# Performance work log

Measured on AMD Instinct MI355X. Metric: run time of the kernel, lower is better.

## Reference

```python
import jax, jax.numpy as jnp
import numpy as np

B, T, C = 4, 2048, 1024   # batch, seq (block_size), n_embd
H, D = 16, 64             # num_heads, head_size (H*D == C)


def setup_inputs() -> dict:
    key = jax.random.key(0)
    ks = jax.random.split(key, 6)
    s = 0.02
    return {
        "x":  jax.random.normal(ks[0], (B, T, C), jnp.float32),
        "Wq": jax.random.normal(ks[1], (H, C, D), jnp.float32) * s,
        "Wk": jax.random.normal(ks[2], (H, C, D), jnp.float32) * s,
        "Wv": jax.random.normal(ks[3], (H, C, D), jnp.float32) * s,
        "Wp": jax.random.normal(ks[4], (C, C), jnp.float32) * s,
        "bp": jnp.zeros((C,), jnp.float32),
        "is_masked": 1,
    }


def reference(x, Wq, Wk, Wv, Wp, bp, is_masked):
    # Batched per-head projections (original loops over H separate Linears)
    q = jnp.einsum("btc,hcd->bhtd", x, Wq)
    k = jnp.einsum("btc,hcd->bhtd", x, Wk)
    v = jnp.einsum("btc,hcd->bhtd", x, Wv)
    # NOTE: original divides by sqrt(C) where C = n_embd (input dim), not head_size
    scores = jnp.einsum("bhtd,bhsd->bhts", q, k) / jnp.sqrt(jnp.asarray(C, x.dtype))
    if is_masked:
        causal = jnp.tril(jnp.ones((T, T), bool))
        scores = jnp.where(causal, scores, jnp.asarray(-jnp.inf, scores.dtype))
    attn = jax.nn.softmax(scores, axis=-1)   # dropout is identity in eval mode
    out = jnp.einsum("bhts,bhsd->bhtd", attn, v)
    # concat heads along the last dim: [B,T,H*D] == [B,T,C]
    out = out.transpose(0, 2, 1, 3).reshape(B, T, C)
    return out @ Wp.T + bp
```

## Files before the change

### kernel.cpp

```cpp
#include <hip/hip_runtime.h>
#include <stdint.h>
#include <type_traits>

typedef unsigned short u16;
typedef unsigned int u32;
typedef __attribute__((ext_vector_type(8))) short frag8;
typedef __attribute__((ext_vector_type(4))) float fx4;
typedef __attribute__((ext_vector_type(16))) float fx16;

#define MFMA(a, b, c) __builtin_amdgcn_mfma_f32_16x16x32_bf16((a), (b), (c), 0, 0, 0)
#define MFMA32(a, b, c) __builtin_amdgcn_mfma_f32_32x32x16_bf16((a), (b), (c), 0, 0, 0)

__device__ __forceinline__ void gload16(const void* g, void* l) {
  __builtin_amdgcn_global_load_lds((const __attribute__((address_space(1))) void*)g,
                                   (__attribute__((address_space(3))) void*)l, 16, 0, 0);
}

__device__ __forceinline__ u16 f2bf(float f) {
  union { float f; unsigned int u; } c; c.f = f;
  unsigned int r = c.u + 0x7FFFu + ((c.u >> 16) & 1u);
  return (u16)(r >> 16);
}

__device__ __forceinline__ u32 cvtpk(float lo, float hi) {
  u32 r;
  asm("v_cvt_pk_bf16_f32 %0, %1, %2" : "=v"(r) : "v"(lo), "v"(hi));
  return r;
}


__global__ __launch_bounds__(256) void cvt_x(const float* __restrict__ x, u16* __restrict__ xb) {
  const int n4 = (8192 * 1024) / 4;
  for (int i = blockIdx.x * 256 + threadIdx.x; i < n4; i += 2048 * 256) {
    float4 v = ((const float4*)x)[i];
    ushort4 o;
    o.x = f2bf(v.x); o.y = f2bf(v.y); o.z = f2bf(v.z); o.w = f2bf(v.w);
    ((ushort4*)xb)[i] = o;
  }
}

__global__ __launch_bounds__(256) void cvt_wqkv(const float* __restrict__ Wq,
                                                const float* __restrict__ Wk,
                                                const float* __restrict__ Wv,
                                                u16* __restrict__ Wt) {
  __shared__ u16 Tls[64][72];
  int hh = blockIdx.x;
  int c0 = blockIdx.y * 64;
  int type = hh >> 4, h = hh & 15;
  const float* Wsrc = (type == 0 ? Wq : (type == 1 ? Wk : Wv)) + (size_t)h * 1024 * 64;
  int t = threadIdx.x;
  int cr = t >> 4, q4 = (t & 15) * 4;
  for (int i = 0; i < 4; ++i) {
    int c = cr + i * 16;
    float4 v = *(const float4*)(Wsrc + (size_t)(c0 + c) * 64 + q4);
    Tls[q4 + 0][c] = f2bf(v.x);
    Tls[q4 + 1][c] = f2bf(v.y);
    Tls[q4 + 2][c] = f2bf(v.z);
    Tls[q4 + 3][c] = f2bf(v.w);
  }
  __syncthreads();
  for (int i = 0; i < 4; ++i) {
    int d = cr + i * 16;
    ushort4 o;
    o.x = Tls[d][q4 + 0]; o.y = Tls[d][q4 + 1]; o.z = Tls[d][q4 + 2]; o.w = Tls[d][q4 + 3];
    *(ushort4*)(Wt + ((size_t)hh * 64 + d) * 1024 + c0 + q4) = o;
  }
}

__global__ __launch_bounds__(256) void cvt_wp(const float* __restrict__ Wp, u16* __restrict__ wb) {
  const int n4 = (1024 * 1024) / 4;
  for (int i = blockIdx.x * 256 + threadIdx.x; i < n4; i += 1024 * 256) {
    float4 v = ((const float4*)Wp)[i];
    ushort4 o;
    o.x = f2bf(v.x); o.y = f2bf(v.y); o.z = f2bf(v.z); o.w = f2bf(v.w);
    ((ushort4*)wb)[i] = o;
  }
}

__global__ __launch_bounds__(256) void transpose_v(const u16* __restrict__ Vb, u16* __restrict__ VTg) {
  __shared__ u16 T[64 * 64];
  int bh = blockIdx.x, t0 = blockIdx.y * 64;
  const u16* src = Vb + ((size_t)bh * 2048 + t0) * 64;
  int tid = threadIdx.x;
  int tl = tid >> 2, c16 = (tid & 3) * 16;
  int swzw = (tl & 7) << 4;
  frag8 a = *(const frag8*)(src + (size_t)tl * 64 + c16);
  frag8 b = *(const frag8*)(src + (size_t)tl * 64 + c16 + 8);
  *(frag8*)((char*)T + tl * 128 + ((c16 * 2) ^ swzw)) = a;
  *(frag8*)((char*)T + tl * 128 + ((c16 * 2 + 16) ^ swzw)) = b;
  __syncthreads();
  int d_ = tid & 63;
#pragma unroll
  for (int k = 0; k < 2; ++k) {
    int c_ = (tid >> 6) + 4 * k;
    frag8 o;
#pragma unroll
    for (int j = 0; j < 8; ++j) {
      int t = c_ * 8 + j;
      o[j] = *(const u16*)((const char*)T + t * 128 + ((2 * d_) ^ ((t & 7) << 4)));
    }
    *(frag8*)(VTg + ((size_t)bh * 64 + d_) * 2048 + t0 + c_ * 8) = o;
  }
}


template <int MODE>
__global__ __launch_bounds__(256) void gemm_bt(const u16* __restrict__ A, const u16* __restrict__ Bw,
                                               u16* __restrict__ Qb, u16* __restrict__ Kb,
                                               u16* __restrict__ Vb, float* __restrict__ outp,
                                               const float* __restrict__ bp) {
  __shared__ u16 As[128 * 32];
  __shared__ u16 Bs[128 * 32];
  int tid = threadIdx.x;
  int m0 = blockIdx.x * 128, n0 = blockIdx.y * 128;
  int wid = tid >> 6, lane = tid & 63, lr = lane & 15, lg = lane >> 4;
  int wm = (wid >> 1) * 64, wn = (wid & 1) * 64;
  const u16* Ag = A + (size_t)m0 * 1024;
  const u16* Bg = Bw + (size_t)n0 * 1024;
  int cidx0 = wid * 2, cidx1 = wid * 2 + 1;
  int rA0 = cidx0 * 16 + (lane >> 2), rA1 = cidx1 * 16 + (lane >> 2);
  int chm = ((lane & 3) ^ ((lane >> 2) & 3)) * 8;
  const u16* Asrc0 = Ag + (size_t)rA0 * 1024 + chm;
  const u16* Asrc1 = Ag + (size_t)rA1 * 1024 + chm;
  const u16* Bsrc0 = Bg + (size_t)rA0 * 1024 + chm;
  const u16* Bsrc1 = Bg + (size_t)rA1 * 1024 + chm;
  u16* lA0 = As + cidx0 * 512; u16* lA1 = As + cidx1 * 512;
  u16* lB0 = Bs + cidx0 * 512; u16* lB1 = Bs + cidx1 * 512;
  int aoff[4], boff[4];
#pragma unroll
  for (int i = 0; i < 4; ++i) {
    aoff[i] = (wm + i * 16 + lr) * 64 + ((lg * 16) ^ ((lr & 3) << 4));
    boff[i] = (wn + i * 16 + lr) * 64 + ((lg * 16) ^ ((lr & 3) << 4));
  }
  fx4 acc[4][4] = {};
  for (int kt = 0; kt < 32; ++kt) {
    __syncthreads();
    gload16(Asrc0 + kt * 32, lA0);
    gload16(Asrc1 + kt * 32, lA1);
    gload16(Bsrc0 + kt * 32, lB0);
    gload16(Bsrc1 + kt * 32, lB1);
    __syncthreads();
    frag8 af[4], bf_[4];
#pragma unroll
    for (int i = 0; i < 4; ++i) af[i] = *(const frag8*)((const char*)As + aoff[i]);
#pragma unroll
    for (int i = 0; i < 4; ++i) bf_[i] = *(const frag8*)((const char*)Bs + boff[i]);
#pragma unroll
    for (int mi = 0; mi < 4; ++mi)
#pragma unroll
      for (int ni = 0; ni < 4; ++ni) acc[mi][ni] = MFMA(af[mi], bf_[ni], acc[mi][ni]);
  }
#pragma unroll
  for (int mi = 0; mi < 4; ++mi)
#pragma unroll
    for (int r = 0; r < 4; ++r) {
      int m = m0 + wm + mi * 16 + lg * 4 + r;
      if (MODE == 0) {
        int b = m >> 11, t = m & 2047;
#pragma unroll
        for (int ni = 0; ni < 4; ++ni) {
          int n = n0 + wn + ni * 16 + lr;
          int type = n >> 10, h = (n >> 6) & 15, d = n & 63;
          u16* dst = (type == 0) ? Qb : ((type == 1) ? Kb : Vb);
          float v = acc[mi][ni][r];
          if (type == 0) v *= 0.04508422002778011f;
          dst[((size_t)(b * 16 + h) * 2048 + t) * 64 + d] = f2bf(v);
        }
      } else {
#pragma unroll
        for (int ni = 0; ni < 4; ++ni) {
          int n = n0 + wn + ni * 16 + lr;
          outp[(size_t)m * 1024 + n] = acc[mi][ni][r] + bp[n];
        }
      }
    }
}


__global__ __launch_bounds__(256, 4) void attn(const u16* __restrict__ Qb, const u16* __restrict__ Kb,
                                               const u16* __restrict__ VTg, u16* __restrict__ Ao,
                                               const int* __restrict__ mflag) {
  __shared__ __align__(16) char LDS[32768];
  const int tid = threadIdx.x, w = tid >> 6, lane = tid & 63;
  const int l31 = lane & 31, hi = lane >> 5;
  const int bh = blockIdx.x;
  const int qt = 15 - (int)blockIdx.y;
  const int masked = mflag[0];
  const int qbase = qt * 128;
  const u16* Qh = Qb + (size_t)bh * (2048 * 64);
  const u16* Kh = Kb + (size_t)bh * (2048 * 64);
  const u16* Vh = VTg + (size_t)bh * (64 * 2048);
  const int qrow = qbase + w * 32 + l31;
  frag8 qf[4];
#pragma unroll
  for (int s = 0; s < 4; ++s) qf[s] = *(const frag8*)(Qh + (size_t)qrow * 64 + s * 16 + hi * 8);
  const int srow = lane >> 3;
  const int schunk = ((lane & 7) ^ srow) * 8;
  const int c0 = w * 2, c1 = w * 2 + 1;
  const u16* kg0 = Kh + (size_t)(c0 * 8 + srow) * 64 + schunk;
  const u16* kg1 = Kh + (size_t)(c1 * 8 + srow) * 64 + schunk;
  const u16* vg0 = Vh + (size_t)(c0 * 8 + srow) * 2048 + schunk;
  const u16* vg1 = Vh + (size_t)(c1 * 8 + srow) * 2048 + schunk;
  const int aK = l31 * 128 + ((hi * 16) ^ ((l31 & 7) << 4));
  const int qmax_w = qbase + w * 32 + 31;
  const int qmin_w = qbase + w * 32;
  float m_run = -__builtin_inff(), l_run = 0.f;
  fx16 oa0 = {}, oa1 = {};
  const int nt = masked ? (2 * qt + 2) : 32;

  auto STAGE = [&](int B, int T) {
    size_t ko = (size_t)T * 4096, vo = (size_t)T * 64;
    gload16(kg0 + ko, LDS + B * 8192 + c0 * 1024);
    gload16(kg1 + ko, LDS + B * 8192 + c1 * 1024);
    gload16(vg0 + vo, LDS + 16384 + B * 8192 + c0 * 1024);
    gload16(vg1 + vo, LDS + 16384 + B * 8192 + c1 * 1024);
  };

  auto TILE = [&](auto Bc, int T) {
    constexpr int B = decltype(Bc)::value;
    if (T + 1 < nt) STAGE(B ^ 1, T + 1);
    bool act = (!masked) || (T * 64 <= qmax_w);
    if (act) {
      fx16 s0v = {}, s1v = {};
#pragma unroll
      for (int ds = 0; ds < 4; ++ds) {
        frag8 k0 = *(const frag8*)(LDS + B * 8192 + (aK ^ (ds << 5)));
        frag8 k1 = *(const frag8*)(LDS + B * 8192 + 4096 + (aK ^ (ds << 5)));
        s0v = MFMA32(k0, qf[ds], s0v);
        s1v = MFMA32(k1, qf[ds], s1v);
      }
      if (masked && T * 64 + 63 > qmin_w) {
#pragma unroll
        for (int g = 0; g < 4; ++g)
#pragma unroll
          for (int r = 0; r < 4; ++r) {
            int sg = T * 64 + r + 8 * g + 4 * hi;
            if (sg > qrow) s0v[4 * g + r] = -__builtin_inff();
            if (sg + 32 > qrow) s1v[4 * g + r] = -__builtin_inff();
          }
      }
      float mx = s0v[0];
#pragma unroll
      for (int i = 1; i < 16; ++i) mx = fmaxf(mx, s0v[i]);
#pragma unroll
      for (int i = 0; i < 16; ++i) mx = fmaxf(mx, s1v[i]);
      mx = fmaxf(mx, __int_as_float(__shfl_xor(__float_as_int(mx), 32)));
      if (!__all(mx <= m_run + 8.0f)) {
        float mn = fmaxf(m_run, mx);
        float al = __builtin_amdgcn_exp2f(m_run - mn);
#pragma unroll
        for (int i = 0; i < 16; ++i) { oa0[i] *= al; oa1[i] *= al; }
        l_run *= al;
        m_run = mn;
      }
      float ps = 0.f;
#pragma unroll
      for (int i = 0; i < 16; ++i) {
        s0v[i] = __builtin_amdgcn_exp2f(s0v[i] - m_run); ps += s0v[i];
      }
#pragma unroll
      for (int i = 0; i < 16; ++i) {
        s1v[i] = __builtin_amdgcn_exp2f(s1v[i] - m_run); ps += s1v[i];
      }
      ps += __int_as_float(__shfl_xor(__float_as_int(ps), 32));
      l_run += ps;
#pragma unroll
      for (int kt = 0; kt < 4; ++kt) {
        const int b8 = (kt & 1) * 8;
        float p0, p1, p2, p3, p4, p5, p6, p7;
        if (kt < 2) { p0=s0v[b8+0];p1=s0v[b8+1];p2=s0v[b8+2];p3=s0v[b8+3];p4=s0v[b8+4];p5=s0v[b8+5];p6=s0v[b8+6];p7=s0v[b8+7]; }
        else        { p0=s1v[b8+0];p1=s1v[b8+1];p2=s1v[b8+2];p3=s1v[b8+3];p4=s1v[b8+4];p5=s1v[b8+5];p6=s1v[b8+6];p7=s1v[b8+7]; }
        u32 X0 = cvtpk(p0, p1), X1 = cvtpk(p2, p3);
        u32 Y0 = cvtpk(p4, p5), Y1 = cvtpk(p6, p7);
        u32 sel0 = hi ? X0 : Y0, sel1 = hi ? X1 : Y1;
        u32 got0 = (u32)__shfl_xor((int)sel0, 32);
        u32 got1 = (u32)__shfl_xor((int)sel1, 32);
        union { u32 u[4]; frag8 f; } pf;
        pf.u[0] = hi ? got0 : X0;
        pf.u[1] = hi ? got1 : X1;
        pf.u[2] = hi ? Y0 : got0;
        pf.u[3] = hi ? Y1 : got1;
        frag8 v0 = *(const frag8*)(LDS + 16384 + B * 8192 + (aK ^ (kt << 5)));
        frag8 v1 = *(const frag8*)(LDS + 16384 + B * 8192 + 4096 + (aK ^ (kt << 5)));
        oa0 = MFMA32(v0, pf.f, oa0);
        oa1 = MFMA32(v1, pf.f, oa1);
      }
    }
    asm volatile("s_waitcnt vmcnt(0)" ::: "memory");
    __builtin_amdgcn_s_barrier();
  };

  STAGE(0, 0);
  asm volatile("s_waitcnt vmcnt(0)" ::: "memory");
  __builtin_amdgcn_s_barrier();
  int t = 0;
  while (true) {
    TILE(std::integral_constant<int, 0>{}, t); ++t; if (t >= nt) break;
    TILE(std::integral_constant<int, 1>{}, t); ++t; if (t >= nt) break;
  }

  float inv = 1.0f / l_run;
  int b = bh >> 4, hh = bh & 15;
  u16* orow = Ao + ((size_t)b * 2048 + qrow) * 1024 + hh * 64;
#pragma unroll
  for (int g = 0; g < 4; ++g) {
    int d0 = 8 * g + 4 * hi;
    u32 wA = cvtpk(oa0[4 * g + 0] * inv, oa0[4 * g + 1] * inv);
    u32 wB = cvtpk(oa0[4 * g + 2] * inv, oa0[4 * g + 3] * inv);
    u32 wC = cvtpk(oa1[4 * g + 0] * inv, oa1[4 * g + 1] * inv);
    u32 wD = cvtpk(oa1[4 * g + 2] * inv, oa1[4 * g + 3] * inv);
    *(u32*)(orow + d0 + 0) = wA;
    *(u32*)(orow + d0 + 2) = wB;
    *(u32*)(orow + d0 + 32) = wC;
    *(u32*)(orow + d0 + 34) = wD;
  }
}


extern "C" void kernel_launch(void* const* d_in, const int* in_sizes, int n_in,
                              void* d_out, int out_size, void* d_ws, size_t ws_size,
                              hipStream_t stream) {
  const float* x = (const float*)d_in[0];
  const float* Wq = (const float*)d_in[1];
  const float* Wk = (const float*)d_in[2];
  const float* Wv = (const float*)d_in[3];
  const float* Wp = (const float*)d_in[4];
  const float* bp = (const float*)d_in[5];
  const int* is_masked = (const int*)d_in[6];
  float* out = (float*)d_out;
  char* ws = (char*)d_ws;
  u16* Xbf = (u16*)(ws + 0);
  u16* Wt  = (u16*)(ws + 16777216);
  u16* Wpb = (u16*)(ws + 23068672);
  u16* Qb  = (u16*)(ws + 25165824);
  u16* Kb  = (u16*)(ws + 41943040);
  u16* Vb  = (u16*)(ws + 58720256);
  u16* Ao  = (u16*)(ws + 75497472);
  u16* VTg = Xbf;

  cvt_x<<<2048, 256, 0, stream>>>(x, Xbf);
  cvt_wqkv<<<dim3(48, 16), 256, 0, stream>>>(Wq, Wk, Wv, Wt);
  cvt_wp<<<1024, 256, 0, stream>>>(Wp, Wpb);
  gemm_bt<0><<<dim3(64, 24), 256, 0, stream>>>(Xbf, Wt, Qb, Kb, Vb, nullptr, nullptr);
  transpose_v<<<dim3(64, 32), 256, 0, stream>>>(Vb, VTg);
  attn<<<dim3(64, 16), 256, 0, stream>>>(Qb, Kb, VTg, Ao, is_masked);
  gemm_bt<1><<<dim3(64, 8), 256, 0, stream>>>(Ao, Wpb, nullptr, nullptr, nullptr, out, bp);
}
```

Before: 168.7 us.

## Replace QKV projection GEMM with 256x192-tile double-buffered 8-wave kernel

The fused QKV projection GEMM moves to a new kernel with 256x192 output tiles, 512 threads, a 64-wide K step and double-buffered LDS filled by direct global-to-LDS loads. Each tile's next K slice is prefetched while MFMAs run, with wave priority raised around the MFMA bursts. Blocks are remapped so neighbouring tiles land on the same XCD, aiming at better L2 reuse. The aim is to raise arithmetic intensity and hide load latency for the biggest GEMM. The cost is 112KB of LDS per block, so fewer blocks fit per CU, and an epilogue with scattered bf16 stores.

```diff
diff --git a/kernel.cpp b/kernel.cpp
--- a/kernel.cpp
+++ b/kernel.cpp
@@ -104,11 +104,115 @@
 }
 
 
-template <int MODE>
-__global__ __launch_bounds__(256) void gemm_bt(const u16* __restrict__ A, const u16* __restrict__ Bw,
-                                               u16* __restrict__ Qb, u16* __restrict__ Kb,
-                                               u16* __restrict__ Vb, float* __restrict__ outp,
-                                               const float* __restrict__ bp) {
+__global__ __launch_bounds__(512, 2) void gemm256(const u16* __restrict__ A, const u16* __restrict__ Bw,
+                                                  u16* __restrict__ Qb, u16* __restrict__ Kb,
+                                                  u16* __restrict__ Vb) {
+  __shared__ __align__(16) char LDSC[114688];
+  const int tid = threadIdx.x, w = tid >> 6, lane = tid & 63;
+  const int lr = lane & 15, lg = lane >> 4;
+  const int wg = blockIdx.x;
+  const int xcd = wg & 7, loc = wg >> 3;
+  const int bx = xcd * 4 + (loc >> 4);
+  const int by = loc & 15;
+  const int m0 = bx * 256, n0 = by * 192;
+  const int r8 = lane >> 3;
+  const int c8 = ((lane & 7) ^ r8) * 8;
+  const u16* aS[4]; const u16* bS[3];
+  char* aD[4]; char* bD[3];
+#pragma unroll
+  for (int l = 0; l < 4; ++l) {
+    aS[l] = A + (size_t)(m0 + l * 64 + w * 8 + r8) * 1024 + c8;
+    aD[l] = LDSC + l * 8192 + w * 1024;
+  }
+#pragma unroll
+  for (int l = 0; l < 3; ++l) {
+    bS[l] = Bw + (size_t)(n0 + l * 64 + w * 8 + r8) * 1024 + c8;
+    bD[l] = LDSC + 65536 + l * 8192 + w * 1024;
+  }
+  const int colX0 = (lg << 4) ^ ((lr & 7) << 4);
+  const int colX1 = ((4 + lg) << 4) ^ ((lr & 7) << 4);
+  const int aRowB = ((w >> 2) * 128 + lr) * 128;
+  const int bRowB = 65536 + ((w & 3) * 48 + lr) * 128;
+
+  fx4 acc[8][3] = {};
+
+#pragma unroll
+  for (int l = 0; l < 4; ++l) gload16(aS[l], aD[l]);
+#pragma unroll
+  for (int l = 0; l < 3; ++l) gload16(bS[l], bD[l]);
+  asm volatile("s_waitcnt vmcnt(0)" ::: "memory");
+  __builtin_amdgcn_s_barrier();
+
+  for (int kt = 0; kt < 16; ++kt) {
+    const int ab = (kt & 1) * 32768;
+    const int bb = (kt & 1) * 24576;
+    frag8 bf2[3][2];
+#pragma unroll
+    for (int p = 0; p < 4; ++p) {
+      if (p == 0) {
+        if (kt + 1 < 16) {
+          const int ko = (kt + 1) * 64;
+          const int ab2 = ab ^ 32768, bb2 = bb ^ 24576;
+#pragma unroll
+          for (int l = 0; l < 4; ++l) gload16(aS[l] + ko, aD[l] + ab2);
+#pragma unroll
+          for (int l = 0; l < 3; ++l) gload16(bS[l] + ko, bD[l] + bb2);
+        }
+#pragma unroll
+        for (int ni = 0; ni < 3; ++ni) {
+          bf2[ni][0] = *(const frag8*)(LDSC + bb + bRowB + ni * 2048 + colX0);
+          bf2[ni][1] = *(const frag8*)(LDSC + bb + bRowB + ni * 2048 + colX1);
+        }
+      }
+      frag8 af2[2][2];
+#pragma unroll
+      for (int dm = 0; dm < 2; ++dm) {
+        af2[dm][0] = *(const frag8*)(LDSC + ab + aRowB + (2 * p + dm) * 2048 + colX0);
+        af2[dm][1] = *(const frag8*)(LDSC + ab + aRowB + (2 * p + dm) * 2048 + colX1);
+      }
+      __builtin_amdgcn_s_barrier();
+      asm volatile("s_waitcnt lgkmcnt(0)" ::: "memory");
+      __builtin_amdgcn_sched_barrier(0);
+      __builtin_amdgcn_s_setprio(1);
+#pragma unroll
+      for (int dm = 0; dm < 2; ++dm)
+#pragma unroll
+        for (int ni = 0; ni < 3; ++ni)
+#pragma unroll
+          for (int ks = 0; ks < 2; ++ks)
+            acc[2 * p + dm][ni] = MFMA(af2[dm][ks], bf2[ni][ks], acc[2 * p + dm][ni]);
+      __builtin_amdgcn_s_setprio(0);
+      __builtin_amdgcn_sched_barrier(0);
+      if (p == 3) {
+        asm volatile("s_waitcnt vmcnt(0)" ::: "memory");
+        __builtin_amdgcn_sched_barrier(0);
+      }
+      __builtin_amdgcn_s_barrier();
+    }
+  }
+
+  const int wmB = (w >> 2) * 128, wnB = (w & 3) * 48;
+#pragma unroll
+  for (int mi = 0; mi < 8; ++mi)
+#pragma unroll
+    for (int r = 0; r < 4; ++r) {
+      int m = m0 + wmB + mi * 16 + lg * 4 + r;
+      int b = m >> 11, t = m & 2047;
+#pragma unroll
+      for (int ni = 0; ni < 3; ++ni) {
+        int n = n0 + wnB + ni * 16 + lr;
+        int type = n >> 10, h = (n >> 6) & 15, d = n & 63;
+        u16* dst = (type == 0) ? Qb : ((type == 1) ? Kb : Vb);
+        float v = acc[mi][ni][r];
+        if (type == 0) v *= 0.04508422002778011f;
+        dst[((size_t)(b * 16 + h) * 2048 + t) * 64 + d] = f2bf(v);
+      }
+    }
+}
+
+
+__global__ __launch_bounds__(256) void gemm_proj(const u16* __restrict__ A, const u16* __restrict__ Bw,
+                                                 float* __restrict__ outp, const float* __restrict__ bp) {
   __shared__ u16 As[128 * 32];
   __shared__ u16 Bs[128 * 32];
   int tid = threadIdx.x;
@@ -155,23 +259,10 @@
 #pragma unroll
     for (int r = 0; r < 4; ++r) {
       int m = m0 + wm + mi * 16 + lg * 4 + r;
-      if (MODE == 0) {
-        int b = m >> 11, t = m & 2047;
-#pragma unroll
-        for (int ni = 0; ni < 4; ++ni) {
-          int n = n0 + wn + ni * 16 + lr;
-          int type = n >> 10, h = (n >> 6) & 15, d = n & 63;
-          u16* dst = (type == 0) ? Qb : ((type == 1) ? Kb : Vb);
-          float v = acc[mi][ni][r];
-          if (type == 0) v *= 0.04508422002778011f;
-          dst[((size_t)(b * 16 + h) * 2048 + t) * 64 + d] = f2bf(v);
-        }
-      } else {
-#pragma unroll
-        for (int ni = 0; ni < 4; ++ni) {
-          int n = n0 + wn + ni * 16 + lr;
-          outp[(size_t)m * 1024 + n] = acc[mi][ni][r] + bp[n];
-        }
+#pragma unroll
+      for (int ni = 0; ni < 4; ++ni) {
+        int n = n0 + wn + ni * 16 + lr;
+        outp[(size_t)m * 1024 + n] = acc[mi][ni][r] + bp[n];
       }
     }
 }
@@ -341,8 +432,8 @@
   cvt_x<<<2048, 256, 0, stream>>>(x, Xbf);
   cvt_wqkv<<<dim3(48, 16), 256, 0, stream>>>(Wq, Wk, Wv, Wt);
   cvt_wp<<<1024, 256, 0, stream>>>(Wp, Wpb);
-  gemm_bt<0><<<dim3(64, 24), 256, 0, stream>>>(Xbf, Wt, Qb, Kb, Vb, nullptr, nullptr);
+  gemm256<<<512, 512, 0, stream>>>(Xbf, Wt, Qb, Kb, Vb);
   transpose_v<<<dim3(64, 32), 256, 0, stream>>>(Vb, VTg);
   attn<<<dim3(64, 16), 256, 0, stream>>>(Qb, Kb, VTg, Ao, is_masked);
-  gemm_bt<1><<<dim3(64, 8), 256, 0, stream>>>(Ao, Wpb, nullptr, nullptr, nullptr, out, bp);
-}
+  gemm_proj<<<dim3(64, 8), 256, 0, stream>>>(Ao, Wpb, out, bp);
+}
```

Result: no change. 166.6 us (-1.3%).

## Rewrite projection GEMMs with larger tiles, multi-stage LDS pipeline and XCD-aware mapping

Applied to the files above, without the earlier changes.

Replaces the 128x128 single-buffered GEMM with a 512-thread kernel using 256xBN tiles and a 64-wide K step. A is double-buffered and B triple-buffered in LDS, with async global-to-LDS loads issued ahead and explicit vmcnt waits and barriers, plus setprio around the MFMA bursts. Workgroups are remapped so neighbouring tiles land on the same XCD to improve L2 reuse. The aim is to hide global load latency and raise data reuse in both the QKV and output projections, at the cost of more LDS per block, which limits occupancy.

```diff
diff --git a/kernel.cpp b/kernel.cpp
--- a/kernel.cpp
+++ b/kernel.cpp
@@ -104,72 +104,124 @@
 }
 
 
-template <int MODE>
-__global__ __launch_bounds__(256) void gemm_bt(const u16* __restrict__ A, const u16* __restrict__ Bw,
-                                               u16* __restrict__ Qb, u16* __restrict__ Kb,
-                                               u16* __restrict__ Vb, float* __restrict__ outp,
-                                               const float* __restrict__ bp) {
-  __shared__ u16 As[128 * 32];
-  __shared__ u16 Bs[128 * 32];
-  int tid = threadIdx.x;
-  int m0 = blockIdx.x * 128, n0 = blockIdx.y * 128;
-  int wid = tid >> 6, lane = tid & 63, lr = lane & 15, lg = lane >> 4;
-  int wm = (wid >> 1) * 64, wn = (wid & 1) * 64;
-  const u16* Ag = A + (size_t)m0 * 1024;
-  const u16* Bg = Bw + (size_t)n0 * 1024;
-  int cidx0 = wid * 2, cidx1 = wid * 2 + 1;
-  int rA0 = cidx0 * 16 + (lane >> 2), rA1 = cidx1 * 16 + (lane >> 2);
-  int chm = ((lane & 3) ^ ((lane >> 2) & 3)) * 8;
-  const u16* Asrc0 = Ag + (size_t)rA0 * 1024 + chm;
-  const u16* Asrc1 = Ag + (size_t)rA1 * 1024 + chm;
-  const u16* Bsrc0 = Bg + (size_t)rA0 * 1024 + chm;
-  const u16* Bsrc1 = Bg + (size_t)rA1 * 1024 + chm;
-  u16* lA0 = As + cidx0 * 512; u16* lA1 = As + cidx1 * 512;
-  u16* lB0 = Bs + cidx0 * 512; u16* lB1 = Bs + cidx1 * 512;
-  int aoff[4], boff[4];
-#pragma unroll
-  for (int i = 0; i < 4; ++i) {
-    aoff[i] = (wm + i * 16 + lr) * 64 + ((lg * 16) ^ ((lr & 3) << 4));
-    boff[i] = (wn + i * 16 + lr) * 64 + ((lg * 16) ^ ((lr & 3) << 4));
-  }
-  fx4 acc[4][4] = {};
-  for (int kt = 0; kt < 32; ++kt) {
-    __syncthreads();
-    gload16(Asrc0 + kt * 32, lA0);
-    gload16(Asrc1 + kt * 32, lA1);
-    gload16(Bsrc0 + kt * 32, lB0);
-    gload16(Bsrc1 + kt * 32, lB1);
-    __syncthreads();
-    frag8 af[4], bf_[4];
-#pragma unroll
-    for (int i = 0; i < 4; ++i) af[i] = *(const frag8*)((const char*)As + aoff[i]);
-#pragma unroll
-    for (int i = 0; i < 4; ++i) bf_[i] = *(const frag8*)((const char*)Bs + boff[i]);
-#pragma unroll
-    for (int mi = 0; mi < 4; ++mi)
-#pragma unroll
-      for (int ni = 0; ni < 4; ++ni) acc[mi][ni] = MFMA(af[mi], bf_[ni], acc[mi][ni]);
-  }
-#pragma unroll
-  for (int mi = 0; mi < 4; ++mi)
+template <int BN, int MODE>
+__global__ __launch_bounds__(512, 2) void gemm2(const u16* __restrict__ A, const u16* __restrict__ Bw,
+                                                u16* __restrict__ Qb, u16* __restrict__ Kb,
+                                                u16* __restrict__ Vb, float* __restrict__ outp,
+                                                const float* __restrict__ bp) {
+  constexpr int NI = BN / 64;
+  constexpr int NB = BN / 64;
+  constexpr int BBYTES = BN * 128;
+  __shared__ __align__(16) char LDSC[65536 + 3 * BBYTES];
+  const int tid = threadIdx.x, w = tid >> 6, lane = tid & 63;
+  const int lr = lane & 15, lg = lane >> 4;
+  constexpr int NBY = (BN == 192) ? 16 : 8;
+  const int wg = blockIdx.x;
+  const int xcd = wg & 7, loc = wg >> 3;
+  const int bx = xcd * 4 + loc / NBY;
+  const int by = loc % NBY;
+  const int m0 = bx * 256, n0 = by * BN;
+  const int r8 = lane >> 3;
+  const int c8 = ((lane & 7) ^ r8) * 8;
+  const u16* aS[4];
+  const u16* bS[NB];
+#pragma unroll
+  for (int l = 0; l < 4; ++l) aS[l] = A + (size_t)(m0 + l * 64 + w * 8 + r8) * 1024 + c8;
+#pragma unroll
+  for (int l = 0; l < NB; ++l) bS[l] = Bw + (size_t)(n0 + l * 64 + w * 8 + r8) * 1024 + c8;
+  const int wmB = (w >> 2) * 128, wnB = (w & 3) * (BN / 4);
+
+  auto rdA = [&](const char* ab, int mi, int ks) -> frag8 {
+    int row = wmB + mi * 16 + lr;
+    return *(const frag8*)(ab + row * 128 + ((((ks << 2) + lg) ^ (lr & 7)) << 4));
+  };
+  auto rdB = [&](const char* bbuf, int ni, int ks) -> frag8 {
+    int row = wnB + ni * 16 + lr;
+    return *(const frag8*)(bbuf + row * 128 + ((((ks << 2) + lg) ^ (lr & 7)) << 4));
+  };
+
+  fx4 acc[8][NI] = {};
+
+#pragma unroll
+  for (int l = 0; l < 4; ++l) gload16(aS[l], LDSC + l * 8192 + w * 1024);
+#pragma unroll
+  for (int l = 0; l < NB; ++l) gload16(bS[l], LDSC + 65536 + l * 8192 + w * 1024);
+#pragma unroll
+  for (int l = 0; l < NB; ++l) gload16(bS[l] + 64, LDSC + 65536 + BBYTES + l * 8192 + w * 1024);
+  if constexpr (NB == 3) asm volatile("s_waitcnt vmcnt(3)" ::: "memory");
+  else asm volatile("s_waitcnt vmcnt(2)" ::: "memory");
+  __builtin_amdgcn_s_barrier();
+
+  for (int t = 0; t < 16; ++t) {
+    const char* ab = LDSC + (t & 1) * 32768;
+    const char* bb = LDSC + 65536 + (t % 3) * BBYTES;
+    char* abN = LDSC + ((t + 1) & 1) * 32768;
+    char* bbN = LDSC + 65536 + ((t + 2) % 3) * BBYTES;
+    frag8 bfr[NI][2];
+#pragma unroll
+    for (int q = 0; q < 4; ++q) {
+      if (q == 0) {
+#pragma unroll
+        for (int ni = 0; ni < NI; ++ni) {
+          bfr[ni][0] = rdB(bb, ni, 0);
+          bfr[ni][1] = rdB(bb, ni, 1);
+        }
+      }
+      frag8 a00 = rdA(ab, 2 * q + 0, 0), a01 = rdA(ab, 2 * q + 0, 1);
+      frag8 a10 = rdA(ab, 2 * q + 1, 0), a11 = rdA(ab, 2 * q + 1, 1);
+      if (q == 0 && t + 1 < 16) {
+#pragma unroll
+        for (int l = 0; l < 4; ++l) gload16(aS[l] + (t + 1) * 64, abN + l * 8192 + w * 1024);
+      }
+      if (q == 2 && t + 2 < 16) {
+        gload16(bS[0] + (t + 2) * 64, bbN + 0 * 8192 + w * 1024);
+        gload16(bS[1] + (t + 2) * 64, bbN + 1 * 8192 + w * 1024);
+      }
+      if (q == 3 && t + 2 < 16 && NB == 3) {
+        gload16(bS[2] + (t + 2) * 64, bbN + 2 * 8192 + w * 1024);
+      }
+      __builtin_amdgcn_s_barrier();
+      __builtin_amdgcn_s_setprio(1);
+#pragma unroll
+      for (int ni = 0; ni < NI; ++ni) {
+        acc[2 * q + 0][ni] = MFMA(a00, bfr[ni][0], acc[2 * q + 0][ni]);
+        acc[2 * q + 0][ni] = MFMA(a01, bfr[ni][1], acc[2 * q + 0][ni]);
+        acc[2 * q + 1][ni] = MFMA(a10, bfr[ni][0], acc[2 * q + 1][ni]);
+        acc[2 * q + 1][ni] = MFMA(a11, bfr[ni][1], acc[2 * q + 1][ni]);
+      }
+      __builtin_amdgcn_s_setprio(0);
+      if (q == 3) {
+        if (t < 14) {
+          if constexpr (NB == 3) asm volatile("s_waitcnt vmcnt(3)" ::: "memory");
+          else asm volatile("s_waitcnt vmcnt(2)" ::: "memory");
+        } else {
+          asm volatile("s_waitcnt vmcnt(0)" ::: "memory");
+        }
+      }
+      __builtin_amdgcn_s_barrier();
+    }
+  }
+
+#pragma unroll
+  for (int mi = 0; mi < 8; ++mi)
 #pragma unroll
     for (int r = 0; r < 4; ++r) {
-      int m = m0 + wm + mi * 16 + lg * 4 + r;
+      int m = m0 + wmB + mi * 16 + lg * 4 + r;
       if (MODE == 0) {
-        int b = m >> 11, t = m & 2047;
-#pragma unroll
-        for (int ni = 0; ni < 4; ++ni) {
-          int n = n0 + wn + ni * 16 + lr;
+        int b = m >> 11, tt = m & 2047;
+#pragma unroll
+        for (int ni = 0; ni < NI; ++ni) {
+          int n = n0 + wnB + ni * 16 + lr;
           int type = n >> 10, h = (n >> 6) & 15, d = n & 63;
           u16* dst = (type == 0) ? Qb : ((type == 1) ? Kb : Vb);
           float v = acc[mi][ni][r];
           if (type == 0) v *= 0.04508422002778011f;
-          dst[((size_t)(b * 16 + h) * 2048 + t) * 64 + d] = f2bf(v);
+          dst[((size_t)(b * 16 + h) * 2048 + tt) * 64 + d] = f2bf(v);
         }
       } else {
 #pragma unroll
-        for (int ni = 0; ni < 4; ++ni) {
-          int n = n0 + wn + ni * 16 + lr;
+        for (int ni = 0; ni < NI; ++ni) {
+          int n = n0 + wnB + ni * 16 + lr;
           outp[(size_t)m * 1024 + n] = acc[mi][ni][r] + bp[n];
         }
       }
@@ -341,8 +393,8 @@
   cvt_x<<<2048, 256, 0, stream>>>(x, Xbf);
   cvt_wqkv<<<dim3(48, 16), 256, 0, stream>>>(Wq, Wk, Wv, Wt);
   cvt_wp<<<1024, 256, 0, stream>>>(Wp, Wpb);
-  gemm_bt<0><<<dim3(64, 24), 256, 0, stream>>>(Xbf, Wt, Qb, Kb, Vb, nullptr, nullptr);
+  gemm2<192, 0><<<512, 512, 0, stream>>>(Xbf, Wt, Qb, Kb, Vb, nullptr, nullptr);
   transpose_v<<<dim3(64, 32), 256, 0, stream>>>(Vb, VTg);
   attn<<<dim3(64, 16), 256, 0, stream>>>(Qb, Kb, VTg, Ao, is_masked);
-  gemm_bt<1><<<dim3(64, 8), 256, 0, stream>>>(Ao, Wpb, nullptr, nullptr, nullptr, out, bp);
-}
+  gemm2<128, 1><<<256, 512, 0, stream>>>(Ao, Wpb, nullptr, nullptr, nullptr, out, bp);
+}
```

Measured after the change: 161.2 us. 4.4% less time.
